# Performance work log

Hardware: AMD Instinct MI355X
Metric: run time of the kernel (lower is better)

Reference implementation:

```python
import jax, jax.numpy as jnp
import numpy as np

ALPHA = 0.9

def setup_inputs() -> dict:
    key = jax.random.key(0)
    k1, k2 = jax.random.split(key)
    x = jax.random.normal(k1, (1024, 32, 1024), dtype=jnp.float32)
    state = jax.random.normal(k2, (32, 1024), dtype=jnp.float32)
    return {"x": x, "state": state}

def reference(x, state):
    # EMA recurrence: s_t = alpha * s_{t-1} + (1 - alpha) * x_t
    def step(s, xt):
        s = xt * (1.0 - ALPHA) + s * ALPHA
        return s, s
    final_state, out = jax.lax.scan(step, state, x)
    return out, final_state
```

## Files before the change

### kernel.cpp

```cpp
#include <hip/hip_runtime.h>


typedef float floatv __attribute__((ext_vector_type(2)));

constexpr int T = 1024;
constexpr int C = 32 * 1024;
constexpr int VEC = 2;
constexpr int CV = C / VEC;
constexpr int CHUNK = 64;
constexpr int NCHUNK = T / CHUNK;
constexpr int WARM = 96;

__global__ __launch_bounds__(256)
void ExponentialDecay_23708219474744_kernel(const float* __restrict__ x,
                                            const float* __restrict__ state,
                                            float* __restrict__ out) {
    const int cv = blockIdx.x * blockDim.x + threadIdx.x;
    const int chunk = blockIdx.y;
    const int t0 = chunk * CHUNK;

    const float a = 0.9f;
    const float oma = 0.1f;

    const floatv* xv = (const floatv*)x;
    floatv* outv = (floatv*)out;

    int tw = t0 - WARM;
    floatv s;
    if (tw <= 0) {
        tw = 0;
        s = ((const floatv*)state)[cv];
    } else {
        s = (floatv)(0.0f);
    }

    #pragma unroll 8
    for (int t = tw; t < t0; ++t) {
        floatv v = xv[(size_t)t * CV + cv];
        s = s * a + v * oma;
    }

    const int t1 = t0 + CHUNK;
    #pragma unroll 8
    for (int t = t0; t < t1; ++t) {
        floatv v = xv[(size_t)t * CV + cv];
        s = s * a + v * oma;
        __builtin_nontemporal_store(s, &outv[(size_t)t * CV + cv]);
    }

    if (chunk == NCHUNK - 1) {
        outv[(size_t)T * CV + cv] = s;
    }
}

extern "C" void kernel_launch(void* const* d_in, const int* in_sizes, int n_in,
                              void* d_out, int out_size, void* d_ws, size_t ws_size,
                              hipStream_t stream) {
    const float* x = (const float*)d_in[0];
    const float* state = (const float*)d_in[1];
    float* out = (float*)d_out;

    dim3 block(256);
    dim3 grid(CV / 256, NCHUNK);
    ExponentialDecay_23708219474744_kernel<<<grid, block, 0, stream>>>(x, state, out);
}
```

Measured before the change: 245.9 us.

## Widen to float4, shorten warmup, and software-pipeline time-step loads

Each thread now handles float4 instead of float2 channels, and the per-chunk warmup is cut from 96 to 64 steps, so less of x is re-read. Loads are issued in groups of 8 time steps with the next group prefetched into registers while the current one is being computed. The goal is to cut redundant read traffic and hide memory latency in this latency-bound scan. In exchange there are half as many threads, so the launch may not fill the GPU. The shorter warmup also leaves a larger truncation error (0.9^64 versus 0.9^96) in the chunk start states.

```diff
diff --git a/kernel.cpp b/kernel.cpp
--- a/kernel.cpp
+++ b/kernel.cpp
@@ -1,15 +1,49 @@
 #include <hip/hip_runtime.h>
 
 
-typedef float floatv __attribute__((ext_vector_type(2)));
+typedef float f4 __attribute__((ext_vector_type(4)));
 
 constexpr int T = 1024;
 constexpr int C = 32 * 1024;
-constexpr int VEC = 2;
-constexpr int CV = C / VEC;
+constexpr int V = 4;
+constexpr int CV = C / V;
 constexpr int CHUNK = 64;
 constexpr int NCHUNK = T / CHUNK;
-constexpr int WARM = 96;
+constexpr int WARM = 64;
+constexpr int U = 8;
+
+template<int STEPS, bool STORE>
+__device__ __forceinline__ void run_steps(const f4* __restrict__ xp,
+                                          f4* __restrict__ op,
+                                          f4& s) {
+    constexpr int NG = STEPS / U;
+    const float a = 0.9f;
+    const float oma = 0.1f;
+
+    f4 cur[U];
+    #pragma unroll
+    for (int i = 0; i < U; ++i) cur[i] = xp[(size_t)i * CV];
+
+    #pragma unroll
+    for (int g = 0; g < NG; ++g) {
+        f4 nxt[U];
+        if (g + 1 < NG) {
+            #pragma unroll
+            for (int i = 0; i < U; ++i)
+                nxt[i] = xp[(size_t)((g + 1) * U + i) * CV];
+        }
+        #pragma unroll
+        for (int i = 0; i < U; ++i) {
+            s = s * a + cur[i] * oma;
+            if (STORE)
+                __builtin_nontemporal_store(s, op + (size_t)(g * U + i) * CV);
+        }
+        if (g + 1 < NG) {
+            #pragma unroll
+            for (int i = 0; i < U; ++i) cur[i] = nxt[i];
+        }
+    }
+}
 
 __global__ __launch_bounds__(256)
 void ExponentialDecay_23708219474744_kernel(const float* __restrict__ x,
@@ -19,37 +53,27 @@
     const int chunk = blockIdx.y;
     const int t0 = chunk * CHUNK;
 
-    const float a = 0.9f;
-    const float oma = 0.1f;
-
-    const floatv* xv = (const floatv*)x;
-    floatv* outv = (floatv*)out;
+    const f4* xv = (const f4*)x;
+    f4* ov = (f4*)out;
 
     int tw = t0 - WARM;
-    floatv s;
+    f4 s;
     if (tw <= 0) {
         tw = 0;
-        s = ((const floatv*)state)[cv];
+        s = ((const f4*)state)[cv];
     } else {
-        s = (floatv)(0.0f);
+        s = (f4)0.0f;
     }
 
-    #pragma unroll 8
-    for (int t = tw; t < t0; ++t) {
-        floatv v = xv[(size_t)t * CV + cv];
-        s = s * a + v * oma;
+    if (chunk > 0) {
+        run_steps<WARM, false>(xv + (size_t)tw * CV + cv, nullptr, s);
     }
 
-    const int t1 = t0 + CHUNK;
-    #pragma unroll 8
-    for (int t = t0; t < t1; ++t) {
-        floatv v = xv[(size_t)t * CV + cv];
-        s = s * a + v * oma;
-        __builtin_nontemporal_store(s, &outv[(size_t)t * CV + cv]);
-    }
+    run_steps<CHUNK, true>(xv + (size_t)t0 * CV + cv,
+                           ov + (size_t)t0 * CV + cv, s);
 
     if (chunk == NCHUNK - 1) {
-        outv[(size_t)T * CV + cv] = s;
+        ov[(size_t)T * CV + cv] = s;
     }
 }
 
```

Measured after the change: 246.1 us. About the same (+0.1%).
